# Performance work log

Hardware: AMD Instinct MI355X
Metric: run time of the kernel (lower is better)

The kernel has to match this reference:

```python
import jax, jax.numpy as jnp
import numpy as np

C = 256
INTER = 32  # C // reduction_ratio(8)
B, H, W = 4, 64, 64


def setup_inputs() -> dict:
    key = jax.random.key(0)
    ks = jax.random.split(key, 8)
    x = jax.random.normal(ks[0], (B, C, H, W), dtype=jnp.float32)
    # 1x1 conv weights stored as [out, in] matrices + biases
    Wq = jax.random.normal(ks[1], (INTER, C), dtype=jnp.float32) * (1.0 / np.sqrt(C))
    bq = jnp.zeros((INTER,), dtype=jnp.float32)
    Wk = jax.random.normal(ks[2], (INTER, C), dtype=jnp.float32) * (1.0 / np.sqrt(C))
    bk = jnp.zeros((INTER,), dtype=jnp.float32)
    Wv = jax.random.normal(ks[3], (C, C), dtype=jnp.float32) * (1.0 / np.sqrt(C))
    bv = jnp.zeros((C,), dtype=jnp.float32)
    gamma = jnp.zeros((1,), dtype=jnp.float32)
    return {"x": x, "Wq": Wq, "bq": bq, "Wk": Wk, "bk": bk, "Wv": Wv, "bv": bv, "gamma": gamma}


def reference(x, Wq, bq, Wk, bk, Wv, bv, gamma):
    b, c, h, w = x.shape
    n = h * w
    xf = x.reshape(b, c, n)  # [B,C,N]
    # 1x1 convs == channel matmuls
    q = jnp.einsum('ic,bcn->bin', Wq, xf) + bq[None, :, None]  # [B,I,N]
    k = jnp.einsum('ic,bcn->bin', Wk, xf) + bk[None, :, None]  # [B,I,N]
    v = jnp.einsum('oc,bcn->bon', Wv, xf) + bv[None, :, None]  # [B,C,N]
    scale = INTER ** (-0.5)
    attn = jnp.einsum('bin,bim->bnm', q, k) * scale  # [B,N,N]
    attn = jax.nn.softmax(attn, axis=-1)
    out = jnp.einsum('bcm,bnm->bcn', v, attn)  # value @ attn^T
    out = out.reshape(b, c, h, w)
    return gamma[0] * out + x
```

## Files before the change

### kernel.cpp

```cpp
#include <hip/hip_runtime.h>
#include <hip/hip_bf16.h>
#include <cstddef>
#include <cstdint>

#define BB 4
#define CC 256
#define II 32
#define NN 4096

#define SCALE_Q 0.25505572751402893f

typedef __attribute__((ext_vector_type(8))) short bf16x8;
typedef __attribute__((ext_vector_type(16))) float f32x16;

static __device__ __forceinline__ int cvt_pk_bf16(float lo, float hi) {
  int d;
  asm("v_cvt_pk_bf16_f32 %0, %1, %2" : "=v"(d) : "v"(lo), "v"(hi));
  return d;
}
static __device__ __forceinline__ void perm32swap_f(float& a, float& b) {
  asm("v_permlane32_swap_b32 %0, %1" : "+v"(a), "+v"(b));
}
static __device__ __forceinline__ float max3f(float a, float b, float c) {
  float d;
  asm("v_max3_f32 %0, %1, %2, %3" : "=v"(d) : "v"(a), "v"(b), "v"(c));
  return d;
}
static __device__ __forceinline__ f32x16 zero16() {
  f32x16 z;
#pragma unroll
  for (int i = 0; i < 16; ++i) z[i] = 0.0f;
  return z;
}
static __device__ __forceinline__ void mfma_bf16_first(bf16x8 a, bf16x8 b, f32x16& c) {
  asm("s_nop 1\n\tv_mfma_f32_32x32x16_bf16 %0, %1, %2, %0"
      : "+v"(c) : "v"(a), "v"(b));
}
static __device__ __forceinline__ void mfma_bf16_last(bf16x8 a, bf16x8 b, f32x16& c) {
  asm("v_mfma_f32_32x32x16_bf16 %0, %1, %2, %0\n\ts_nop 7\n\ts_nop 7"
      : "+v"(c) : "v"(a), "v"(b));
}
static __device__ __forceinline__ bf16x8 pack8(float f0, float f1, float f2,
    float f3, float f4, float f5, float f6, float f7) {
  union { int w[4]; bf16x8 v8; } u;
  u.w[0] = cvt_pk_bf16(f0, f1);
  u.w[1] = cvt_pk_bf16(f2, f3);
  u.w[2] = cvt_pk_bf16(f4, f5);
  u.w[3] = cvt_pk_bf16(f6, f7);
  return u.v8;
}
static __device__ __forceinline__ ushort f2bfu(float f) {
  union { __hip_bfloat16 h; ushort u; } cv;
  cv.h = __float2bfloat16(f);
  return cv.u;
}
static __device__ __forceinline__ int pack4_fp8(float a, float b, float c, float d) {
  int r = __builtin_amdgcn_cvt_pk_fp8_f32(a, b, 0, false);
  r = __builtin_amdgcn_cvt_pk_fp8_f32(c, d, r, true);
  return r;
}
static __device__ __forceinline__ unsigned char f2fp8(float f) {
  return (unsigned char)(__builtin_amdgcn_cvt_pk_fp8_f32(f, f, 0, false) & 0xff);
}


__global__ __launch_bounds__(64, 3) void proj_mfma(
    const float* __restrict__ Wq, const float* __restrict__ bq,
    const float* __restrict__ Wk, const float* __restrict__ bk,
    const float* __restrict__ Wv, const float* __restrict__ bv,
    const float* __restrict__ x,
    ushort* __restrict__ qT, ushort* __restrict__ kT,
    unsigned char* __restrict__ vT8) {
  const int lane = threadIdx.x;
  const int l31 = lane & 31;
  const int h = lane >> 5;
  const int b = blockIdx.x;
  const int n0 = blockIdx.y * 32;
  const int og = blockIdx.z;

  const float* xb = x + (size_t)b * CC * NN + n0 + l31;
  const float* wr0 = (og == 0) ? (Wq + (size_t)l31 * CC)
                               : (Wv + (size_t)((og - 1) * 64 + l31) * CC);
  const float* wr1 = (og == 0) ? (Wk + (size_t)l31 * CC)
                               : (Wv + (size_t)((og - 1) * 64 + 32 + l31) * CC);

  f32x16 acc0 = zero16(), acc1 = zero16();
#pragma unroll 4
  for (int ks = 0; ks < 16; ++ks) {
    const int c = ks * 16 + h * 8;
    const float* xp = xb + (size_t)c * NN;
    bf16x8 xf = pack8(xp[0], xp[(size_t)1 * NN], xp[(size_t)2 * NN],
                      xp[(size_t)3 * NN], xp[(size_t)4 * NN], xp[(size_t)5 * NN],
                      xp[(size_t)6 * NN], xp[(size_t)7 * NN]);
    float4 wa = *(const float4*)(wr0 + c);
    float4 wb = *(const float4*)(wr0 + c + 4);
    bf16x8 wf0 = pack8(wa.x, wa.y, wa.z, wa.w, wb.x, wb.y, wb.z, wb.w);
    float4 wc = *(const float4*)(wr1 + c);
    float4 wd = *(const float4*)(wr1 + c + 4);
    bf16x8 wf1 = pack8(wc.x, wc.y, wc.z, wc.w, wd.x, wd.y, wd.z, wd.w);
    acc0 = __builtin_amdgcn_mfma_f32_32x32x16_bf16(wf0, xf, acc0, 0, 0, 0);
    acc1 = __builtin_amdgcn_mfma_f32_32x32x16_bf16(wf1, xf, acc1, 0, 0, 0);
  }

  if (og == 0) {
    ushort* qb = qT + (size_t)(b * 128 + (n0 >> 5)) * 1024;
    ushort* kb = kT + (size_t)(b * 128 + (n0 >> 5)) * 1024;
#pragma unroll
    for (int r = 0; r < 16; ++r) {
      const int i = (r & 3) + 8 * (r >> 2) + 4 * h;
      const size_t off = (size_t)(i >> 4) * 512 + ((i >> 3) & 1) * 256 + 8 * l31 + (i & 7);
      qb[off] = f2bfu((acc0[r] + bq[i]) * SCALE_Q);
      kb[off] = f2bfu(acc1[r] + bk[i]);
    }
  } else {
    const int n = n0 + l31;
    const size_t nsub = (size_t)(n >> 4) * 512 + ((size_t)((n >> 3) & 1)) * 256 + (n & 7);
    const size_t bbase = (size_t)b * (1 << 20);
#pragma unroll
    for (int r = 0; r < 16; ++r) {
      const int rp = (r & 3) + 8 * (r >> 2) + 4 * h;
      const int c0 = (og - 1) * 64 + rp;
      const int c1 = c0 + 32;
      vT8[bbase + (size_t)(c0 >> 5) * 131072 + nsub + (c0 & 31) * 8] = f2fp8(acc0[r] + bv[c0]);
      vT8[bbase + (size_t)(c1 >> 5) * 131072 + nsub + (c1 & 31) * 8] = f2fp8(acc1[r] + bv[c1]);
    }
  }
}

__global__ __launch_bounds__(512, 4) void flash_coop(
    const ushort* __restrict__ qT, const ushort* __restrict__ kT,
    const unsigned char* __restrict__ vT8, const float* __restrict__ x,
    const float* __restrict__ gamma, float* __restrict__ out) {
  __shared__ __align__(16) unsigned char pbuf[2][32 * 264];
  __shared__ float mlds[264];
  __shared__ float slds[264];

  const int tid = threadIdx.x;
  const int lane = tid & 63;
  const int w = tid >> 6;
  const int q = lane & 31;
  const int h = lane >> 5;

  const int wg = blockIdx.x;
  const int xcd = wg & 7;
  const int b = xcd >> 1;
  const int nt = ((xcd & 1) << 6) + (wg >> 3);
  const int n0 = nt * 32;

  const ushort* qb = qT + (size_t)(b * 128 + nt) * 1024 + lane * 8;
  const bf16x8 qf0 = *reinterpret_cast<const bf16x8*>(qb);
  const bf16x8 qf1 = *reinterpret_cast<const bf16x8*>(qb + 512);

  const ushort* ktb = kT + (size_t)b * 128 * 1024;
  const unsigned char* vtb = vT8 + (size_t)b * (1 << 20) + (size_t)w * 131072 + lane * 8;

  f32x16 accA = zero16(), accB = zero16();
  float m_run = -1e30f, l_run = 0.0f;
  long vregA[8], vregB[8];

  {
    const ushort* kc = ktb + (size_t)(0 * 8 + w) * 1024 + lane * 8;
    const bf16x8 kf0 = *reinterpret_cast<const bf16x8*>(kc);
    const bf16x8 kf1 = *reinterpret_cast<const bf16x8*>(kc + 512);
    f32x16 st = zero16();
    mfma_bf16_first(kf0, qf0, st);
    mfma_bf16_last(kf1, qf1, st);

#pragma unroll
    for (int kp = 0; kp < 8; ++kp) {
      vregA[kp] = *reinterpret_cast<const long*>(vtb + (2 * kp) * 512);
      vregB[kp] = *reinterpret_cast<const long*>(vtb + (2 * kp + 1) * 512);
    }

    float m0 = max3f(st[0], st[1], st[2]);
    float m1 = max3f(st[3], st[4], st[5]);
    float m2 = max3f(st[6], st[7], st[8]);
    float m3 = max3f(st[9], st[10], st[11]);
    m0 = max3f(st[12], st[13], m0);
    m1 = max3f(st[14], st[15], m1);
    float mx = max3f(m0, m1, fmaxf(m2, m3));
    float sw1 = mx, sw2 = mx;
    perm32swap_f(sw1, sw2);
    if (lane < 32) mlds[w * 33 + q] = fmaxf(sw1, sw2);
    __syncthreads();
    float tmax = mlds[q];
#pragma unroll
    for (int i = 1; i < 8; ++i) tmax = fmaxf(tmax, mlds[i * 33 + q]);
    m_run = tmax;

#pragma unroll
    for (int r = 0; r < 16; ++r) st[r] = __builtin_amdgcn_exp2f(st[r] - m_run);
    float s0 = ((st[0] + st[1]) + (st[2] + st[3])) +
               ((st[4] + st[5]) + (st[6] + st[7]));
    float s1 = ((st[8] + st[9]) + (st[10] + st[11])) +
               ((st[12] + st[13]) + (st[14] + st[15]));
    float pssum = s0 + s1;
    float pa = pssum, pb = pssum;
    perm32swap_f(pa, pb);
    if (lane < 32) slds[w * 33 + q] = pa + pb;
#pragma unroll
    for (int rg = 0; rg < 4; ++rg) {
      const int pk = pack4_fp8(st[rg * 4], st[rg * 4 + 1], st[rg * 4 + 2], st[rg * 4 + 3]);
      *reinterpret_cast<int*>(&pbuf[0][q * 264 + w * 32 + rg * 8 + h * 4]) = pk;
    }
    __syncthreads();
    float tsum = slds[q];
#pragma unroll
    for (int i = 1; i < 8; ++i) tsum += slds[i * 33 + q];
    l_run = tsum;
  }

  for (int t = 1; t < 16; ++t) {
    const int pv = t - 1;
    const int pcur = pv & 1;
    const int pnext = t & 1;

    const ushort* kc = ktb + (size_t)(t * 8 + w) * 1024 + lane * 8;
    const bf16x8 kf0 = *reinterpret_cast<const bf16x8*>(kc);
    const bf16x8 kf1 = *reinterpret_cast<const bf16x8*>(kc + 512);

    const unsigned char* pb = &pbuf[pcur][q * 264 + h * 8];
    __builtin_amdgcn_s_setprio(1);
    long pA = *reinterpret_cast<const long*>(pb);
    long pB = *reinterpret_cast<const long*>(pb + 16);
#pragma unroll
    for (int kp = 0; kp < 8; ++kp) {
      long pAn = 0, pBn = 0;
      if (kp < 7) {
        pAn = *reinterpret_cast<const long*>(pb + (2 * kp + 2) * 16);
        pBn = *reinterpret_cast<const long*>(pb + (2 * kp + 3) * 16);
      }
      accA = __builtin_amdgcn_mfma_f32_32x32x16_fp8_fp8(vregA[kp], pA, accA, 0, 0, 0);
      accB = __builtin_amdgcn_mfma_f32_32x32x16_fp8_fp8(vregB[kp], pB, accB, 0, 0, 0);
      pA = pAn; pB = pBn;
    }

    const unsigned char* vcn = vtb + (size_t)(t * 16) * 512;
#pragma unroll
    for (int kp = 0; kp < 8; ++kp) {
      vregA[kp] = *reinterpret_cast<const long*>(vcn + (2 * kp) * 512);
      vregB[kp] = *reinterpret_cast<const long*>(vcn + (2 * kp + 1) * 512);
    }

    f32x16 st = zero16();
    mfma_bf16_first(kf0, qf0, st);
    mfma_bf16_last(kf1, qf1, st);
    __builtin_amdgcn_s_setprio(0);

    float m0 = max3f(st[0], st[1], st[2]);
    float m1 = max3f(st[3], st[4], st[5]);
    float m2 = max3f(st[6], st[7], st[8]);
    float m3 = max3f(st[9], st[10], st[11]);
    m0 = max3f(st[12], st[13], m0);
    m1 = max3f(st[14], st[15], m1);
    float mx = max3f(m0, m1, fmaxf(m2, m3));
    float sw1 = mx, sw2 = mx;
    perm32swap_f(sw1, sw2);
    if (lane < 32) mlds[w * 33 + q] = fmaxf(sw1, sw2);
    __syncthreads();
    float tmax = mlds[q];
#pragma unroll
    for (int i = 1; i < 8; ++i) tmax = fmaxf(tmax, mlds[i * 33 + q]);

    if (__any(tmax > m_run + 8.0f)) {
      const float mnew = fmaxf(m_run, tmax);
      const float f = __builtin_amdgcn_exp2f(m_run - mnew);
#pragma unroll
      for (int r = 0; r < 16; ++r) { accA[r] *= f; accB[r] *= f; }
      l_run *= f;
      m_run = mnew;
    }

#pragma unroll
    for (int r = 0; r < 16; ++r) st[r] = __builtin_amdgcn_exp2f(st[r] - m_run);
    float s0 = ((st[0] + st[1]) + (st[2] + st[3])) +
               ((st[4] + st[5]) + (st[6] + st[7]));
    float s1 = ((st[8] + st[9]) + (st[10] + st[11])) +
               ((st[12] + st[13]) + (st[14] + st[15]));
    float pssum = s0 + s1;
    float pa = pssum, pb2 = pssum;
    perm32swap_f(pa, pb2);
    if (lane < 32) slds[w * 33 + q] = pa + pb2;

#pragma unroll
    for (int rg = 0; rg < 4; ++rg) {
      const int pk = pack4_fp8(st[rg * 4], st[rg * 4 + 1], st[rg * 4 + 2], st[rg * 4 + 3]);
      *reinterpret_cast<int*>(&pbuf[pnext][q * 264 + w * 32 + rg * 8 + h * 4]) = pk;
    }
    __syncthreads();

    float tsum = slds[q];
#pragma unroll
    for (int i = 1; i < 8; ++i) tsum += slds[i * 33 + q];
    l_run += tsum;
  }

  {
    const unsigned char* pb = &pbuf[1][q * 264 + h * 8];
    __builtin_amdgcn_s_setprio(1);
#pragma unroll
    for (int kp = 0; kp < 8; ++kp) {
      const long pA = *reinterpret_cast<const long*>(pb + (2 * kp) * 16);
      const long pB = *reinterpret_cast<const long*>(pb + (2 * kp + 1) * 16);
      accA = __builtin_amdgcn_mfma_f32_32x32x16_fp8_fp8(vregA[kp], pA, accA, 0, 0, 0);
      accB = __builtin_amdgcn_mfma_f32_32x32x16_fp8_fp8(vregB[kp], pB, accB, 0, 0, 0);
    }
    __builtin_amdgcn_s_setprio(0);
  }

  const float g = gamma[0];
  const float linv = 1.0f / l_run;
#pragma unroll
  for (int r = 0; r < 16; ++r) {
    const int c = w * 32 + (r & 3) + 8 * (r >> 2) + 4 * h;
    const size_t idx = ((size_t)b * CC + c) * NN + n0 + q;
    out[idx] = g * (accA[r] + accB[r]) * linv + x[idx];
  }
}

extern "C" void kernel_launch(void* const* d_in, const int* in_sizes, int n_in,
                              void* d_out, int out_size, void* d_ws, size_t ws_size,
                              hipStream_t stream) {
  const float* x = (const float*)d_in[0];
  const float* Wq = (const float*)d_in[1];
  const float* bq = (const float*)d_in[2];
  const float* Wk = (const float*)d_in[3];
  const float* bk = (const float*)d_in[4];
  const float* Wv = (const float*)d_in[5];
  const float* bv = (const float*)d_in[6];
  const float* gamma = (const float*)d_in[7];
  float* out = (float*)d_out;

  ushort* qT = (ushort*)d_ws;
  ushort* kT = qT + (size_t)BB * 128 * 1024;
  unsigned char* vT8 = (unsigned char*)(kT + (size_t)BB * 128 * 1024);

  proj_mfma<<<dim3(BB, NN / 32, 5), dim3(64), 0, stream>>>(
      Wq, bq, Wk, bk, Wv, bv, x, qT, kT, vT8);
  flash_coop<<<dim3(512), dim3(512), 0, stream>>>(
      qT, kT, vT8, x, gamma, out);
}
```

Measured before the change: 77.42 us.

## Share x tile in LDS across five output-group waves in projection kernel

The projection kernel used to launch five separate single-wave blocks per (batch, 32-column) tile, and each block re-read the same x slice from global memory with strided scalar loads. Now one 320-thread block stages the 256x32 x tile into shared memory once with float4 loads, and each of its five waves computes one output group (q/k or a 64-channel slice of v) reading x from LDS. This removes the 5x redundant global reads of x and improves load coalescing. The cost is a 32KB LDS allocation, a block-wide barrier, and fewer, larger blocks, which may reduce occupancy.

```diff
diff --git a/kernel.cpp b/kernel.cpp
--- a/kernel.cpp
+++ b/kernel.cpp
@@ -64,34 +64,45 @@
 }
 
 
-__global__ __launch_bounds__(64, 3) void proj_mfma(
+__global__ __launch_bounds__(320, 2) void proj_lds(
     const float* __restrict__ Wq, const float* __restrict__ bq,
     const float* __restrict__ Wk, const float* __restrict__ bk,
     const float* __restrict__ Wv, const float* __restrict__ bv,
     const float* __restrict__ x,
     ushort* __restrict__ qT, ushort* __restrict__ kT,
     unsigned char* __restrict__ vT8) {
-  const int lane = threadIdx.x;
+  __shared__ float xs[256 * 32];
+
+  const int tid = threadIdx.x;
+  const int w = tid >> 6;
+  const int lane = tid & 63;
   const int l31 = lane & 31;
   const int h = lane >> 5;
   const int b = blockIdx.x;
   const int n0 = blockIdx.y * 32;
-  const int og = blockIdx.z;
-
-  const float* xb = x + (size_t)b * CC * NN + n0 + l31;
-  const float* wr0 = (og == 0) ? (Wq + (size_t)l31 * CC)
-                               : (Wv + (size_t)((og - 1) * 64 + l31) * CC);
-  const float* wr1 = (og == 0) ? (Wk + (size_t)l31 * CC)
-                               : (Wv + (size_t)((og - 1) * 64 + 32 + l31) * CC);
+
+  {
+    const float* xb = x + (size_t)b * CC * NN + n0;
+    for (int i = w; i < 32; i += 5) {
+      const float* src = xb + (size_t)(i * 8 + (lane >> 3)) * NN + (lane & 7) * 4;
+      const float4 v = *(const float4*)src;
+      *(float4*)&xs[i * 256 + lane * 4] = v;
+    }
+  }
+  __syncthreads();
+
+  const float* wr0 = (w == 0) ? (Wq + (size_t)l31 * CC)
+                              : (Wv + (size_t)((w - 1) * 64 + l31) * CC);
+  const float* wr1 = (w == 0) ? (Wk + (size_t)l31 * CC)
+                              : (Wv + (size_t)((w - 1) * 64 + 32 + l31) * CC);
 
   f32x16 acc0 = zero16(), acc1 = zero16();
 #pragma unroll 4
   for (int ks = 0; ks < 16; ++ks) {
     const int c = ks * 16 + h * 8;
-    const float* xp = xb + (size_t)c * NN;
-    bf16x8 xf = pack8(xp[0], xp[(size_t)1 * NN], xp[(size_t)2 * NN],
-                      xp[(size_t)3 * NN], xp[(size_t)4 * NN], xp[(size_t)5 * NN],
-                      xp[(size_t)6 * NN], xp[(size_t)7 * NN]);
+    const float* xp = &xs[c * 32 + l31];
+    bf16x8 xf = pack8(xp[0], xp[32], xp[64], xp[96],
+                      xp[128], xp[160], xp[192], xp[224]);
     float4 wa = *(const float4*)(wr0 + c);
     float4 wb = *(const float4*)(wr0 + c + 4);
     bf16x8 wf0 = pack8(wa.x, wa.y, wa.z, wa.w, wb.x, wb.y, wb.z, wb.w);
@@ -102,7 +113,7 @@
     acc1 = __builtin_amdgcn_mfma_f32_32x32x16_bf16(wf1, xf, acc1, 0, 0, 0);
   }
 
-  if (og == 0) {
+  if (w == 0) {
     ushort* qb = qT + (size_t)(b * 128 + (n0 >> 5)) * 1024;
     ushort* kb = kT + (size_t)(b * 128 + (n0 >> 5)) * 1024;
 #pragma unroll
@@ -119,7 +130,7 @@
 #pragma unroll
     for (int r = 0; r < 16; ++r) {
       const int rp = (r & 3) + 8 * (r >> 2) + 4 * h;
-      const int c0 = (og - 1) * 64 + rp;
+      const int c0 = (w - 1) * 64 + rp;
       const int c1 = c0 + 32;
       vT8[bbase + (size_t)(c0 >> 5) * 131072 + nsub + (c0 & 31) * 8] = f2fp8(acc0[r] + bv[c0]);
       vT8[bbase + (size_t)(c1 >> 5) * 131072 + nsub + (c1 & 31) * 8] = f2fp8(acc1[r] + bv[c1]);
@@ -335,7 +346,7 @@
   ushort* kT = qT + (size_t)BB * 128 * 1024;
   unsigned char* vT8 = (unsigned char*)(kT + (size_t)BB * 128 * 1024);
 
-  proj_mfma<<<dim3(BB, NN / 32, 5), dim3(64), 0, stream>>>(
+  proj_lds<<<dim3(BB, NN / 32), dim3(320), 0, stream>>>(
       Wq, bq, Wk, bk, Wv, bv, x, qT, kT, vT8);
   flash_coop<<<dim3(512), dim3(512), 0, stream>>>(
       qT, kT, vT8, x, gamma, out);
```

Measured after the change: 73.65 us. 4.9% less time.
